# Kernel tuning notes

Measured on AMD Instinct MI355X. Metric: run time of the kernel, lower is better.

## Reference

```python
import jax, jax.numpy as jnp
import numpy as np

N = 100000   # num nodes
E = 1200000  # num edges (before self-loops)
K = 2        # SGConv propagation hops


def _gcn_norm(edge_index, edge_weight):
    # PyG gcn_norm: add self-loops (weight 1) then symmetric normalization
    loop = jnp.arange(N, dtype=edge_index.dtype)
    src = jnp.concatenate([edge_index[0], loop])
    dst = jnp.concatenate([edge_index[1], loop])
    w = jnp.concatenate([edge_weight, jnp.ones((N,), edge_weight.dtype)])
    deg = jax.ops.segment_sum(w, dst, num_segments=N)
    dinv = jnp.where(deg > 0, jax.lax.rsqrt(deg), jnp.zeros_like(deg))
    norm = dinv[src] * w * dinv[dst]
    return src, dst, norm


def _sgconv(x, src, dst, norm, W, b):
    # K hops of A_hat @ x, then linear: x @ W.T + b
    for _ in range(K):
        x = jax.ops.segment_sum(norm[:, None] * x[src], dst, num_segments=N)
    return x @ W.T + b


def setup_inputs() -> dict:
    key = jax.random.key(0)
    k = jax.random.split(key, 6)
    d_in, d_hid, d_out = 64, 64, 40
    x = jax.random.normal(k[0], (N, d_in), jnp.float32)
    edge_index = jax.random.randint(k[1], (2, E), 0, N, jnp.int32)
    edge_weight = jnp.ones((E,), jnp.float32)
    W1 = jax.random.normal(k[2], (d_hid, d_in), jnp.float32) / np.sqrt(d_in)
    b1 = jnp.zeros((d_hid,), jnp.float32)
    W2 = jax.random.normal(k[3], (d_out, d_hid), jnp.float32) / np.sqrt(d_hid)
    b2 = jnp.zeros((d_out,), jnp.float32)
    return {"x": x, "edge_index": edge_index, "edge_weight": edge_weight,
            "W1": W1, "b1": b1, "W2": W2, "b2": b2}


def reference(x, edge_index, edge_weight, W1, b1, W2, b2):
    # eval mode: F.dropout(p=0.6, training=False) is identity
    src, dst, norm = _gcn_norm(edge_index, edge_weight)
    h = jax.nn.relu(_sgconv(x, src, dst, norm, W1, b1))
    out = _sgconv(h, src, dst, norm, W2, b2)
    return out
```

## Files before the change

### kernel.cpp

```cpp
#include <hip/hip_runtime.h>
#include <hip/hip_fp16.h>


#define SCAN_TPB 256
#define SCAN_ITEMS 8
#define SCAN_CHUNK (SCAN_TPB * SCAN_ITEMS)
#define P1_EDGES 2048
#define MAX_NB 784


__global__ __launch_bounds__(SCAN_TPB) void scan_partial_kernel(const int* __restrict__ cnt,
                                                                int* __restrict__ bsums, int N_) {
    int t = threadIdx.x;
    int base = blockIdx.x * SCAN_CHUNK + t * SCAN_ITEMS;
    int s = 0;
    #pragma unroll
    for (int j = 0; j < SCAN_ITEMS; ++j) { int i = base + j; if (i < N_) s += cnt[i]; }
    __shared__ int sm[SCAN_TPB];
    sm[t] = s; __syncthreads();
    for (int o = SCAN_TPB / 2; o > 0; o >>= 1) {
        if (t < o) sm[t] += sm[t + o];
        __syncthreads();
    }
    if (t == 0) bsums[blockIdx.x] = sm[0];
}

__global__ __launch_bounds__(1024) void scan_bsums_kernel(int* bsums, int nb,
                                                          int* out, int N_) {
    __shared__ int sm[1024];
    int t = threadIdx.x;
    int v = (t < nb) ? bsums[t] : 0;
    sm[t] = v; __syncthreads();
    for (int o = 1; o < 1024; o <<= 1) {
        int u = (t >= o) ? sm[t - o] : 0;
        __syncthreads();
        sm[t] += u;
        __syncthreads();
    }
    if (t < nb) bsums[t] = sm[t] - v;
    if (t == 1023) out[N_] = sm[1023];
}

__global__ __launch_bounds__(SCAN_TPB) void scan_final_kernel(const int* __restrict__ cnt,
                                                              const int* __restrict__ bsums,
                                                              int* __restrict__ out, int N_) {
    int t = threadIdx.x;
    int base = blockIdx.x * SCAN_CHUNK + t * SCAN_ITEMS;
    int loc[SCAN_ITEMS];
    int s = 0;
    #pragma unroll
    for (int j = 0; j < SCAN_ITEMS; ++j) {
        int i = base + j;
        int c = (i < N_) ? cnt[i] : 0;
        loc[j] = s; s += c;
    }
    __shared__ int sm[SCAN_TPB];
    sm[t] = s; __syncthreads();
    for (int o = 1; o < SCAN_TPB; o <<= 1) {
        int u = (t >= o) ? sm[t - o] : 0;
        __syncthreads();
        sm[t] += u;
        __syncthreads();
    }
    int excl = bsums[blockIdx.x] + sm[t] - s;
    #pragma unroll
    for (int j = 0; j < SCAN_ITEMS; ++j) {
        int i = base + j;
        if (i < N_) out[i] = excl + loc[j];
    }
}

__global__ __launch_bounds__(256) void p1_count_kernel(const int* __restrict__ ei,
                                                       int* __restrict__ coarseCnt,
                                                       int E_, int PB, int NB) {
    __shared__ int hist[MAX_NB];
    int tid = threadIdx.x;
    for (int u = tid; u < NB; u += 256) hist[u] = 0;
    __syncthreads();
    int base = blockIdx.x * P1_EDGES;
    #pragma unroll
    for (int j = 0; j < P1_EDGES / 512; ++j) {
        int e = base + j * 512 + tid * 2;
        if (e + 1 < E_) {
            int2 d2 = *(const int2*)&ei[E_ + e];
            atomicAdd(&hist[d2.x >> 7], 1);
            atomicAdd(&hist[d2.y >> 7], 1);
        } else if (e < E_) {
            atomicAdd(&hist[ei[E_ + e] >> 7], 1);
        }
    }
    __syncthreads();
    for (int u = tid; u < NB; u += 256) coarseCnt[u * PB + blockIdx.x] = hist[u];
}

__global__ __launch_bounds__(256) void p1_scatter_kernel(const int* __restrict__ ei,
                                                         const float* __restrict__ w,
                                                         const int* __restrict__ coarseOff,
                                                         int2* __restrict__ sorted,
                                                         int E_, int PB, int NB) {
    __shared__ int lcur[MAX_NB];
    int tid = threadIdx.x;
    for (int u = tid; u < NB; u += 256) lcur[u] = coarseOff[u * PB + blockIdx.x];
    __syncthreads();
    int base = blockIdx.x * P1_EDGES;
    #pragma unroll
    for (int j = 0; j < P1_EDGES / 512; ++j) {
        int e = base + j * 512 + tid * 2;
        if (e + 1 < E_) {
            int2   s2 = *(const int2*)&ei[e];
            int2   d2 = *(const int2*)&ei[E_ + e];
            float2 w2 = *(const float2*)&w[e];
            int p0 = atomicAdd(&lcur[d2.x >> 7], 1);
            sorted[p0] = make_int2(s2.x | ((d2.x & 127) << 17), __float_as_int(w2.x));
            int p1 = atomicAdd(&lcur[d2.y >> 7], 1);
            sorted[p1] = make_int2(s2.y | ((d2.y & 127) << 17), __float_as_int(w2.y));
        } else if (e < E_) {
            int dst = ei[E_ + e];
            int pos = atomicAdd(&lcur[dst >> 7], 1);
            sorted[pos] = make_int2(ei[e] | ((dst & 127) << 17), __float_as_int(w[e]));
        }
    }
}

__global__ __launch_bounds__(256) void p2_fine_kernel(const int2* __restrict__ sorted,
                                                      const int* __restrict__ coarseOff,
                                                      int2* __restrict__ edge,
                                                      int* __restrict__ row_ptr,
                                                      float* __restrict__ dinv,
                                                      int N_, int E_, int PB, int NB) {
    __shared__ int fcnt[128], fexc[128], fcur[128];
    __shared__ float fdeg[128];
    const int b = blockIdx.x;
    const int tid = threadIdx.x;
    const int start = coarseOff[b * PB];
    const int end = (b + 1 < NB) ? coarseOff[(b + 1) * PB] : E_;
    if (tid < 128) { fcnt[tid] = 0; fdeg[tid] = 1.0f; }
    __syncthreads();
    for (int p = start + tid; p < end; p += 256)
        atomicAdd(&fcnt[sorted[p].x >> 17], 1);
    __syncthreads();
    if (tid < 128) fexc[tid] = fcnt[tid];
    __syncthreads();
    for (int o = 1; o < 128; o <<= 1) {
        int v = (tid < 128 && tid >= o) ? fexc[tid - o] : 0;
        __syncthreads();
        if (tid < 128) fexc[tid] += v;
        __syncthreads();
    }
    const int node0 = b << 7;
    if (tid < 128) {
        fexc[tid] -= fcnt[tid];
        fcur[tid] = 0;
        int node = node0 + tid;
        if (node < N_) row_ptr[node] = start + fexc[tid];
    }
    __syncthreads();
    for (int p = start + tid; p < end; p += 256) {
        int2 pk = sorted[p];
        int fine = pk.x >> 17;
        int src  = pk.x & 0x1FFFF;
        int r = atomicAdd(&fcur[fine], 1);
        atomicAdd(&fdeg[fine], __int_as_float(pk.y));
        edge[start + fexc[fine] + r] = make_int2(src, pk.y);
    }
    __syncthreads();
    if (tid < 128) {
        int node = node0 + tid;
        if (node < N_) {
            float s = fdeg[tid];
            dinv[node] = (s > 0.f) ? (1.0f / sqrtf(s)) : 0.f;
        }
    }
    if (b == 0 && tid == 0) row_ptr[N_] = E_;
}

__global__ __launch_bounds__(256) void scale_csr_kernel(int2* __restrict__ edge,
                                                        const int* __restrict__ row_ptr,
                                                        const float* __restrict__ dinv, int N_) {
    int n = blockIdx.x * blockDim.x + threadIdx.x;
    if (n < N_) {
        float dd = dinv[n];
        int p0 = row_ptr[n], p1 = row_ptr[n + 1];
        for (int p = p0; p < p1; ++p) {
            int2 e = edge[p];
            edge[p].y = __float_as_int(__int_as_float(e.y) * dinv[e.x] * dd);
        }
    }
}

#define FMA_MIX_LO(accv, hbits, vw) \
    asm("v_fma_mix_f32 %0, %1, %2, %0 op_sel_hi:[1,0,0]" : "+v"(accv) : "v"(hbits), "v"(vw))
#define FMA_MIX_HI(accv, hbits, vw) \
    asm("v_fma_mix_f32 %0, %1, %2, %0 op_sel:[1,0,0] op_sel_hi:[1,0,0]" : "+v"(accv) : "v"(hbits), "v"(vw))

template<int NL, int EPI>
__global__ __launch_bounds__(256) void hop_h_kernel(const __half* __restrict__ xin,
                                                    void* __restrict__ xout,
                                                    const float* __restrict__ dinv,
                                                    const int* __restrict__ row_ptr,
                                                    const int2* __restrict__ edge,
                                                    const float* __restrict__ bias, int N_) {
    int wave = (blockIdx.x * blockDim.x + threadIdx.x) >> 6;
    int lane = threadIdx.x & 63;
    if (wave >= N_) return;
    const int d   = wave;
    const int g4  = lane >> 4;
    const int hl  = lane & 15;
    const int hle = (NL == 16) ? hl : min(hl, NL - 1);

    int e0 = row_ptr[d], e1 = row_ptr[d + 1];
    int nE = e1 - e0;
    float di = dinv[d];
    float2 selfv = ((const float2*)(xin + (size_t)d * 64))[hle];
    float acc[4] = {0.f, 0.f, 0.f, 0.f};

    for (int eb = 0; eb < nE; eb += 64) {
        bool ok = (eb + lane) < nE;
        int2 ev = ok ? edge[e0 + eb + lane] : make_int2(d, 0);
        int m = min(64, nE - eb);
        for (int g = 0; g < m; g += 8) {
            int   s0 = __shfl(ev.x, g + g4);
            int   s1 = __shfl(ev.x, g + 4 + g4);
            float v0 = __shfl(__int_as_float(ev.y), g + g4);
            float v1 = __shfl(__int_as_float(ev.y), g + 4 + g4);
            float2 x0 = ((const float2*)(xin + (size_t)s0 * 64))[hle];
            float2 x1 = ((const float2*)(xin + (size_t)s1 * 64))[hle];
            FMA_MIX_LO(acc[0], x0.x, v0); FMA_MIX_HI(acc[1], x0.x, v0);
            FMA_MIX_LO(acc[2], x0.y, v0); FMA_MIX_HI(acc[3], x0.y, v0);
            FMA_MIX_LO(acc[0], x1.x, v1); FMA_MIX_HI(acc[1], x1.x, v1);
            FMA_MIX_LO(acc[2], x1.y, v1); FMA_MIX_HI(acc[3], x1.y, v1);
        }
    }
    #pragma unroll
    for (int u = 0; u < 4; ++u) {
        acc[u] += __shfl_xor(acc[u], 16);
        acc[u] += __shfl_xor(acc[u], 32);
    }
    float dii = di * di;
    FMA_MIX_LO(acc[0], selfv.x, dii); FMA_MIX_HI(acc[1], selfv.x, dii);
    FMA_MIX_LO(acc[2], selfv.y, dii); FMA_MIX_HI(acc[3], selfv.y, dii);

    if (lane < NL) {
        if constexpr (EPI == 0) {
            float2 pk;
            ((__half2*)&pk)[0] = __floats2half2_rn(acc[0], acc[1]);
            ((__half2*)&pk)[1] = __floats2half2_rn(acc[2], acc[3]);
            ((float2*)((__half*)xout + (size_t)d * 64))[lane] = pk;
        } else if constexpr (EPI == 1) {
            float4 bv = ((const float4*)bias)[lane];
            float2 pk;
            ((__half2*)&pk)[0] = __floats2half2_rn(fmaxf(acc[0] + bv.x, 0.f),
                                                   fmaxf(acc[1] + bv.y, 0.f));
            ((__half2*)&pk)[1] = __floats2half2_rn(fmaxf(acc[2] + bv.z, 0.f),
                                                   fmaxf(acc[3] + bv.w, 0.f));
            ((float2*)((__half*)xout + (size_t)d * 64))[lane] = pk;
        } else {
            float4 bv = ((const float4*)bias)[lane];
            float4 r = make_float4(acc[0] + bv.x, acc[1] + bv.y,
                                   acc[2] + bv.z, acc[3] + bv.w);
            *(float4*)((float*)xout + (size_t)d * 40 + lane * 4) = r;
        }
    }
}

template<int F, bool INH>
__global__ __launch_bounds__(256, 4) void linear_tiled_kernel(const void* __restrict__ hin,
                                                              __half* __restrict__ outp,
                                                              const float* __restrict__ W,
                                                              int N_) {
    constexpr int BM = 64;
    __shared__ float hs[BM * 64];
    __shared__ float ws[64 * 64];
    const int tid  = threadIdx.x;
    const int base = blockIdx.x * BM;

    for (int u = tid; u < 64 * 16; u += 256) {
        int f = u >> 4, kc = u & 15;
        float4 v = (f < F) ? ((const float4*)W)[f * 16 + kc]
                           : make_float4(0.f, 0.f, 0.f, 0.f);
        *(float4*)&ws[f * 64 + ((kc ^ ((f >> 2) & 7)) << 2)] = v;
    }
    const int lim = min(BM, N_ - base);
    for (int u = tid; u < BM * 16; u += 256) {
        int n = u >> 4, kc = u & 15;
        float4 v;
        if (n < lim) {
            if constexpr (INH) {
                float2 hv = ((const float2*)((const __half*)hin + (size_t)(base + n) * 64))[kc];
                const __half2* hh = (const __half2*)&hv;
                float2 a = __half22float2(hh[0]);
                float2 b = __half22float2(hh[1]);
                v = make_float4(a.x, a.y, b.x, b.y);
            } else {
                v = ((const float4*)((const float*)hin + (size_t)(base + n) * 64))[kc];
            }
        } else v = make_float4(0.f, 0.f, 0.f, 0.f);
        *(float4*)&hs[n * 64 + ((kc ^ ((n >> 2) & 7)) << 2)] = v;
    }
    __syncthreads();

    const int f0 = (tid & 15) << 2;
    const int n0 = (tid >> 4) << 2;
    float4 acc[4];
    #pragma unroll
    for (int i = 0; i < 4; ++i) acc[i] = make_float4(0.f, 0.f, 0.f, 0.f);

    #pragma unroll 2
    for (int kc = 0; kc < 16; ++kc) {
        float4 hv[4], wv[4];
        #pragma unroll
        for (int i = 0; i < 4; ++i) {
            int n = n0 + i;
            hv[i] = *(const float4*)&hs[n * 64 + ((kc ^ ((n >> 2) & 7)) << 2)];
        }
        #pragma unroll
        for (int j = 0; j < 4; ++j) {
            int f = f0 + j;
            wv[j] = *(const float4*)&ws[f * 64 + ((kc ^ ((f >> 2) & 7)) << 2)];
        }
        #pragma unroll
        for (int i = 0; i < 4; ++i) {
            acc[i].x = fmaf(hv[i].x, wv[0].x, acc[i].x);
            acc[i].x = fmaf(hv[i].y, wv[0].y, acc[i].x);
            acc[i].x = fmaf(hv[i].z, wv[0].z, acc[i].x);
            acc[i].x = fmaf(hv[i].w, wv[0].w, acc[i].x);
            acc[i].y = fmaf(hv[i].x, wv[1].x, acc[i].y);
            acc[i].y = fmaf(hv[i].y, wv[1].y, acc[i].y);
            acc[i].y = fmaf(hv[i].z, wv[1].z, acc[i].y);
            acc[i].y = fmaf(hv[i].w, wv[1].w, acc[i].y);
            acc[i].z = fmaf(hv[i].x, wv[2].x, acc[i].z);
            acc[i].z = fmaf(hv[i].y, wv[2].y, acc[i].z);
            acc[i].z = fmaf(hv[i].z, wv[2].z, acc[i].z);
            acc[i].z = fmaf(hv[i].w, wv[2].w, acc[i].z);
            acc[i].w = fmaf(hv[i].x, wv[3].x, acc[i].w);
            acc[i].w = fmaf(hv[i].y, wv[3].y, acc[i].w);
            acc[i].w = fmaf(hv[i].z, wv[3].z, acc[i].w);
            acc[i].w = fmaf(hv[i].w, wv[3].w, acc[i].w);
        }
    }

    if (f0 < F) {
        #pragma unroll
        for (int i = 0; i < 4; ++i) {
            int n = base + n0 + i;
            if (n < N_) {
                __half* o = outp + (size_t)n * 64 + f0;
                ((__half2*)o)[0] = __floats2half2_rn(acc[i].x, acc[i].y);
                ((__half2*)o)[1] = __floats2half2_rn(acc[i].z, acc[i].w);
            }
        }
    }
}

extern "C" void kernel_launch(void* const* d_in, const int* in_sizes, int n_in,
                              void* d_out, int out_size, void* d_ws, size_t ws_size,
                              hipStream_t stream) {
    const float* x   = (const float*)d_in[0];
    const int*   ei  = (const int*)d_in[1];
    const float* w   = (const float*)d_in[2];
    const float* W1  = (const float*)d_in[3];
    const float* b1  = (const float*)d_in[4];
    const float* W2  = (const float*)d_in[5];
    const float* b2  = (const float*)d_in[6];
    float* out = (float*)d_out;

    const int N_ = in_sizes[0] / 64;
    const int E_ = in_sizes[2];
    const int PB = (E_ + P1_EDGES - 1) / P1_EDGES;
    const int NB = (N_ + 127) >> 7;
    const int M  = NB * PB;

    char* ws = (char*)d_ws;
    size_t off = 0;
    auto alloc = [&](size_t bytes) { size_t o = off; off += (bytes + 255) & ~(size_t)255; return o; };
    float* dinv      = (float*)(ws + alloc((size_t)N_ * 4));
    int*   row_ptr   = (int*)  (ws + alloc(((size_t)N_ + 1) * 4));
    int*   bsums     = (int*)  (ws + alloc(1024 * 4));
    int*   coarseCnt = (int*)  (ws + alloc((size_t)M * 4));
    int*   coarseOff = (int*)  (ws + alloc(((size_t)M + 1) * 4));
    int2*  edge      = (int2*) (ws + alloc((size_t)E_ * 8));
    float* bufA      = (float*)(ws + alloc((size_t)N_ * 64 * 4));
    float* bufB      = (float*)(ws + alloc((size_t)N_ * 64 * 4));
    int2*   sorted = (int2*)bufA;
    __half* hA0    = (__half*)bufA;
    __half* hLo    = (__half*)bufB;
    __half* hHi    = (__half*)((char*)bufB + (size_t)N_ * 64 * 2);
    (void)ws_size; (void)n_in; (void)out_size;

    const int bn = (N_ + 255) / 256;
    const int bh = (N_ + 3) / 4;
    const int nbs = (M + SCAN_CHUNK - 1) / SCAN_CHUNK;
    const int bl_ = (N_ + 63) / 64;

    p1_count_kernel<<<PB, 256, 0, stream>>>(ei, coarseCnt, E_, PB, NB);
    scan_partial_kernel<<<nbs, SCAN_TPB, 0, stream>>>(coarseCnt, bsums, M);
    scan_bsums_kernel<<<1, 1024, 0, stream>>>(bsums, nbs, coarseOff, M);
    scan_final_kernel<<<nbs, SCAN_TPB, 0, stream>>>(coarseCnt, bsums, coarseOff, M);
    p1_scatter_kernel<<<PB, 256, 0, stream>>>(ei, w, coarseOff, sorted, E_, PB, NB);
    p2_fine_kernel<<<NB, 256, 0, stream>>>(sorted, coarseOff, edge, row_ptr, dinv, N_, E_, PB, NB);
    scale_csr_kernel<<<bn, 256, 0, stream>>>(edge, row_ptr, dinv, N_);

    linear_tiled_kernel<64, false><<<bl_, 256, 0, stream>>>(x, hLo, W1, N_);
    hop_h_kernel<16, 0><<<bh, 256, 0, stream>>>(hLo, hHi, dinv, row_ptr, edge, nullptr, N_);
    hop_h_kernel<16, 1><<<bh, 256, 0, stream>>>(hHi, hA0, dinv, row_ptr, edge, b1, N_);
    linear_tiled_kernel<40, true><<<bl_, 256, 0, stream>>>(hA0, hLo, W2, N_);
    hop_h_kernel<10, 0><<<bh, 256, 0, stream>>>(hLo, hHi, dinv, row_ptr, edge, nullptr, N_);
    hop_h_kernel<10, 2><<<bh, 256, 0, stream>>>(hHi, out, dinv, row_ptr, edge, b2, N_);
}
```

Before: 247.1 us.

## Map four destination nodes per wavefront in hop gather kernel

The hop kernel now assigns each 16-lane quarter of a wavefront to its own destination node instead of spreading one node's edges across four lane groups. This removes the cross-group shuffle reduction and quarters the number of wavefronts launched. Each group loads up to 16 edges at a time and loops to the maximum degree among the four nodes, so degree imbalance within a wave adds idle iterations. Fewer independent gathers are in flight per node, but more nodes are processed in parallel.

After: 221.9 us. -10.2%, faster.

```diff
diff --git a/kernel.cpp b/kernel.cpp
--- a/kernel.cpp
+++ b/kernel.cpp
@@ -202,27 +202,33 @@
                                                     const float* __restrict__ bias, int N_) {
     int wave = (blockIdx.x * blockDim.x + threadIdx.x) >> 6;
     int lane = threadIdx.x & 63;
-    if (wave >= N_) return;
-    const int d   = wave;
-    const int g4  = lane >> 4;
+    const int g   = lane >> 4;
     const int hl  = lane & 15;
     const int hle = (NL == 16) ? hl : min(hl, NL - 1);
 
-    int e0 = row_ptr[d], e1 = row_ptr[d + 1];
-    int nE = e1 - e0;
+    int nd = wave * 4 + g;
+    bool real = nd < N_;
+    int d = real ? nd : (N_ - 1);
+
+    int e0 = row_ptr[d];
+    int nE = real ? (row_ptr[d + 1] - e0) : 0;
     float di = dinv[d];
     float2 selfv = ((const float2*)(xin + (size_t)d * 64))[hle];
     float acc[4] = {0.f, 0.f, 0.f, 0.f};
 
-    for (int eb = 0; eb < nE; eb += 64) {
-        bool ok = (eb + lane) < nE;
-        int2 ev = ok ? edge[e0 + eb + lane] : make_int2(d, 0);
-        int m = min(64, nE - eb);
-        for (int g = 0; g < m; g += 8) {
-            int   s0 = __shfl(ev.x, g + g4);
-            int   s1 = __shfl(ev.x, g + 4 + g4);
-            float v0 = __shfl(__int_as_float(ev.y), g + g4);
-            float v1 = __shfl(__int_as_float(ev.y), g + 4 + g4);
+    int maxNE = nE;
+    maxNE = max(maxNE, __shfl_xor(maxNE, 16));
+    maxNE = max(maxNE, __shfl_xor(maxNE, 32));
+
+    for (int eb = 0; eb < maxNE; eb += 16) {
+        int rem = nE - eb;
+        int2 ev = (hl < rem) ? edge[e0 + eb + hl] : make_int2(d, 0);
+        int mm = min(16, maxNE - eb);
+        for (int j = 0; j < mm; j += 2) {
+            int   s0 = __shfl(ev.x, (g << 4) | j);
+            int   s1 = __shfl(ev.x, (g << 4) | (j + 1));
+            float v0 = __shfl(__int_as_float(ev.y), (g << 4) | j);
+            float v1 = __shfl(__int_as_float(ev.y), (g << 4) | (j + 1));
             float2 x0 = ((const float2*)(xin + (size_t)s0 * 64))[hle];
             float2 x1 = ((const float2*)(xin + (size_t)s1 * 64))[hle];
             FMA_MIX_LO(acc[0], x0.x, v0); FMA_MIX_HI(acc[1], x0.x, v0);
@@ -231,34 +237,29 @@
             FMA_MIX_LO(acc[2], x1.y, v1); FMA_MIX_HI(acc[3], x1.y, v1);
         }
     }
-    #pragma unroll
-    for (int u = 0; u < 4; ++u) {
-        acc[u] += __shfl_xor(acc[u], 16);
-        acc[u] += __shfl_xor(acc[u], 32);
-    }
     float dii = di * di;
     FMA_MIX_LO(acc[0], selfv.x, dii); FMA_MIX_HI(acc[1], selfv.x, dii);
     FMA_MIX_LO(acc[2], selfv.y, dii); FMA_MIX_HI(acc[3], selfv.y, dii);
 
-    if (lane < NL) {
+    if (real && hl < NL) {
         if constexpr (EPI == 0) {
             float2 pk;
             ((__half2*)&pk)[0] = __floats2half2_rn(acc[0], acc[1]);
             ((__half2*)&pk)[1] = __floats2half2_rn(acc[2], acc[3]);
-            ((float2*)((__half*)xout + (size_t)d * 64))[lane] = pk;
+            ((float2*)((__half*)xout + (size_t)d * 64))[hl] = pk;
         } else if constexpr (EPI == 1) {
-            float4 bv = ((const float4*)bias)[lane];
+            float4 bv = ((const float4*)bias)[hl];
             float2 pk;
             ((__half2*)&pk)[0] = __floats2half2_rn(fmaxf(acc[0] + bv.x, 0.f),
                                                    fmaxf(acc[1] + bv.y, 0.f));
             ((__half2*)&pk)[1] = __floats2half2_rn(fmaxf(acc[2] + bv.z, 0.f),
                                                    fmaxf(acc[3] + bv.w, 0.f));
-            ((float2*)((__half*)xout + (size_t)d * 64))[lane] = pk;
+            ((float2*)((__half*)xout + (size_t)d * 64))[hl] = pk;
         } else {
-            float4 bv = ((const float4*)bias)[lane];
+            float4 bv = ((const float4*)bias)[hl];
             float4 r = make_float4(acc[0] + bv.x, acc[1] + bv.y,
                                    acc[2] + bv.z, acc[3] + bv.w);
-            *(float4*)((float*)xout + (size_t)d * 40 + lane * 4) = r;
+            *(float4*)((float*)xout + (size_t)d * 40 + hl * 4) = r;
         }
     }
 }
@@ -388,7 +389,7 @@
     (void)ws_size; (void)n_in; (void)out_size;
 
     const int bn = (N_ + 255) / 256;
-    const int bh = (N_ + 3) / 4;
+    const int bh4 = (N_ + 15) / 16;
     const int nbs = (M + SCAN_CHUNK - 1) / SCAN_CHUNK;
     const int bl_ = (N_ + 63) / 64;
 
@@ -401,9 +402,9 @@
     scale_csr_kernel<<<bn, 256, 0, stream>>>(edge, row_ptr, dinv, N_);
 
     linear_tiled_kernel<64, false><<<bl_, 256, 0, stream>>>(x, hLo, W1, N_);
-    hop_h_kernel<16, 0><<<bh, 256, 0, stream>>>(hLo, hHi, dinv, row_ptr, edge, nullptr, N_);
-    hop_h_kernel<16, 1><<<bh, 256, 0, stream>>>(hHi, hA0, dinv, row_ptr, edge, b1, N_);
+    hop_h_kernel<16, 0><<<bh4, 256, 0, stream>>>(hLo, hHi, dinv, row_ptr, edge, nullptr, N_);
+    hop_h_kernel<16, 1><<<bh4, 256, 0, stream>>>(hHi, hA0, dinv, row_ptr, edge, b1, N_);
     linear_tiled_kernel<40, true><<<bl_, 256, 0, stream>>>(hA0, hLo, W2, N_);
-    hop_h_kernel<10, 0><<<bh, 256, 0, stream>>>(hLo, hHi, dinv, row_ptr, edge, nullptr, N_);
-    hop_h_kernel<10, 2><<<bh, 256, 0, stream>>>(hHi, out, dinv, row_ptr, edge, b2, N_);
-}
+    hop_h_kernel<10, 0><<<bh4, 256, 0, stream>>>(hLo, hHi, dinv, row_ptr, edge, nullptr, N_);
+    hop_h_kernel<10, 2><<<bh4, 256, 0, stream>>>(hHi, out, dinv, row_ptr, edge, b2, N_);
+}
```
